# Kernel optimization log

Measured on AMD Instinct MI355X. Metric: run time of the kernel, lower is better.

The kernel has to match this reference:

```python
import jax, jax.numpy as jnp
import numpy as np

NUM_HEADS = 16
D_MODEL = 1024
HEAD_DIM = D_MODEL // NUM_HEADS
SCALE = float(np.sqrt(HEAD_DIM))  # NOTE: original multiplies q by sqrt(head_dim)
EPS = 1e-5


def layernorm(x, g, b):
    # LayerNorm over last dim (head_dim), learnable affine
    mu = jnp.mean(x, axis=-1, keepdims=True)
    var = jnp.mean(jnp.square(x - mu), axis=-1, keepdims=True)
    return (x - mu) * jax.lax.rsqrt(var + EPS) * g + b


def setup_inputs() -> dict:
    key = jax.random.key(0)
    ks = jax.random.split(key, 8)
    B, Nq, Nc = 2, 2048, 2048
    s = 0.02
    return {
        "x_query": jax.random.normal(ks[0], (B, Nq, D_MODEL), jnp.float32),
        "x_context": jax.random.normal(ks[1], (B, Nc, D_MODEL), jnp.float32),
        "Wq": jax.random.normal(ks[2], (D_MODEL, D_MODEL), jnp.float32) * s,
        "Wkv": jax.random.normal(ks[3], (D_MODEL, 2 * D_MODEL), jnp.float32) * s,
        "Wp": jax.random.normal(ks[4], (D_MODEL, D_MODEL), jnp.float32) * s,
        "bp": jnp.zeros((D_MODEL,), jnp.float32),
        "ln_g": jnp.ones((HEAD_DIM,), jnp.float32),
        "ln_b": jnp.zeros((HEAD_DIM,), jnp.float32),
    }


def reference(x_query, x_context, Wq, Wkv, Wp, bp, ln_g, ln_b):
    B, Nq, _ = x_query.shape
    Nc = x_context.shape[1]
    H, D = NUM_HEADS, HEAD_DIM
    # projections
    q = (x_query @ Wq).reshape(B, Nq, H, D).transpose(0, 2, 1, 3)  # b h n d
    kv = (x_context @ Wkv).reshape(B, Nc, 2, H, D)
    k = kv[:, :, 0].transpose(0, 2, 1, 3)  # b h n d
    v = kv[:, :, 1].transpose(0, 2, 1, 3)
    # QK-LayerNorm (shared params)
    q = layernorm(q, ln_g, ln_b)
    k = layernorm(k, ln_g, ln_b)
    # NOTE: faithful to source — q is MULTIPLIED by sqrt(head_dim)
    q = q * SCALE
    attn = jnp.einsum("bhqd,bhkd->bhqk", q, k)
    attn = jax.nn.softmax(attn, axis=-1)
    out = jnp.einsum("bhqk,bhkd->bhqd", attn, v)
    out = out.transpose(0, 2, 1, 3).reshape(B, Nq, H * D)
    return out @ Wp + bp
```

## Files before the change

kernel.cpp:

```cpp
#include <hip/hip_runtime.h>
#include <stdint.h>

#define NUM_HEADS 16
#define HEAD_DIM 64
#define D_MODEL 1024
#define SEQ 2048
#define BATCH 2

typedef unsigned short u16;
typedef _Float16 f16x8 __attribute__((ext_vector_type(8)));
typedef float f32x4 __attribute__((ext_vector_type(4)));

__device__ __forceinline__ u16 f2h(float f) {
    _Float16 h = (_Float16)f;
    return __builtin_bit_cast(u16, h);
}
__device__ __forceinline__ float h2f(u16 h) {
    return (float)__builtin_bit_cast(_Float16, h);
}
__device__ __forceinline__ uint32_t pkrtz(float a, float b) {
    return __builtin_bit_cast(uint32_t, __builtin_amdgcn_cvt_pkrtz(a, b));
}
__device__ __forceinline__ uint32_t pkrtn(float a, float b) {
    return (uint32_t)f2h(a) | ((uint32_t)f2h(b) << 16);
}

__device__ __forceinline__ float ex2(float x) {
#if __has_builtin(__builtin_amdgcn_exp2f)
    return __builtin_amdgcn_exp2f(x);
#else
    float r;
    asm("v_exp_f32 %0, %1" : "=v"(r) : "v"(x));
    return r;
#endif
}

__device__ __forceinline__ f16x8 ld8h(const u16* p) {
    return *reinterpret_cast<const f16x8*>(p);
}

__device__ __forceinline__ void gl_lds16(const void* g, void* l) {
    __builtin_amdgcn_global_load_lds(
        (const __attribute__((address_space(1))) void*)g,
        (__attribute__((address_space(3))) void*)l,
        16, 0, 0);
}

template <int CTRL>
__device__ __forceinline__ float dpp_mov(float x) {
    return __builtin_bit_cast(float,
        __builtin_amdgcn_update_dpp(0, __builtin_bit_cast(int, x), CTRL, 0xf, 0xf, true));
}
__device__ __forceinline__ float rowsum16(float x) {
    x += dpp_mov<0x121>(x);
    x += dpp_mov<0x122>(x);
    x += dpp_mov<0x124>(x);
    x += dpp_mov<0x128>(x);
    return x;
}

__global__ __launch_bounds__(256) void k_prep(const float* __restrict__ xq,
                                              const float* __restrict__ xc,
                                              const float* __restrict__ Wq,
                                              const float* __restrict__ Wkv,
                                              const float* __restrict__ Wp,
                                              u16* __restrict__ xq16,
                                              u16* __restrict__ xc16,
                                              u16* __restrict__ WqT16,
                                              u16* __restrict__ WkvT16,
                                              u16* __restrict__ WpT16) {
    __shared__ float tile[32][33];
    const int t = blockIdx.x;
    if (t < 8192) {
        int i = t * 256 + threadIdx.x;
        const float* src; u16* dst; int j;
        if (i < 1048576) { src = xq; dst = xq16; j = i; }
        else             { src = xc; dst = xc16; j = i - 1048576; }
        float4 v = reinterpret_cast<const float4*>(src)[j];
        ushort4 o;
        o.x = f2h(v.x); o.y = f2h(v.y); o.z = f2h(v.z); o.w = f2h(v.w);
        reinterpret_cast<ushort4*>(dst)[j] = o;
        return;
    }
    const float* W; u16* WT; int N, bi;
    if (t < 9216)       { W = Wq;  WT = WqT16;  N = 1024; bi = t - 8192; }
    else if (t < 11264) { W = Wkv; WT = WkvT16; N = 2048; bi = t - 9216; }
    else                { W = Wp;  WT = WpT16;  N = 1024; bi = t - 11264; }
    const int K = 1024;
    const int nb = N / 32;
    const int bn = (bi % nb) * 32, bk = (bi / nb) * 32;
    const int tx = threadIdx.x & 31;
    const int ty = threadIdx.x >> 5;
#pragma unroll
    for (int i = 0; i < 32; i += 8)
        tile[ty + i][tx] = W[(size_t)(bk + ty + i) * N + bn + tx];
    __syncthreads();
#pragma unroll
    for (int i = 0; i < 32; i += 8)
        WT[(size_t)(bn + ty + i) * K + bk + tx] = f2h(tile[tx][ty + i]);
}

__device__ __forceinline__ void gemm_mainloop_f16(const u16* __restrict__ A,
                                                  const u16* __restrict__ Bt,
                                                  u16* As, u16* Bs,
                                                  int tileM, int tileN, int K,
                                                  f32x4 acc[4][4]) {
    const int tid = threadIdx.x;
    const int lane = tid & 63;
    const int wv = tid >> 6;
    const int wm = wv >> 1, wn = wv & 1;
    const int quad = lane >> 4, l15 = lane & 15;

    const int c0 = tid, c1 = tid + 256;
    const u16* Ap0 = A + (size_t)(tileM + (c0 >> 2)) * K + (c0 & 3) * 8;
    const u16* Ap1 = A + (size_t)(tileM + (c1 >> 2)) * K + (c1 & 3) * 8;
    const u16* Bp0 = Bt + (size_t)(tileN + (c0 >> 2)) * K + (c0 & 3) * 8;
    const u16* Bp1 = Bt + (size_t)(tileN + (c1 >> 2)) * K + (c1 & 3) * 8;

    gl_lds16(Ap0, &As[c0 * 8]);
    gl_lds16(Ap1, &As[c1 * 8]);
    gl_lds16(Bp0, &Bs[c0 * 8]);
    gl_lds16(Bp1, &Bs[c1 * 8]);

    for (int k0 = 0; k0 < K; k0 += 32) {
        __syncthreads();
        const int cb = (k0 >> 5) & 1;
        if (k0 + 32 < K) {
            const int nbuf = cb ^ 1;
            gl_lds16(Ap0 + k0 + 32, &As[nbuf * 4096 + c0 * 8]);
            gl_lds16(Ap1 + k0 + 32, &As[nbuf * 4096 + c1 * 8]);
            gl_lds16(Bp0 + k0 + 32, &Bs[nbuf * 4096 + c0 * 8]);
            gl_lds16(Bp1 + k0 + 32, &Bs[nbuf * 4096 + c1 * 8]);
        }
        const int cbo = cb * 4096;
        f16x8 af[4], bfr[4];
#pragma unroll
        for (int mi = 0; mi < 4; ++mi)
            af[mi] = ld8h(&As[cbo + (wm * 64 + mi * 16 + l15) * 32 + quad * 8]);
#pragma unroll
        for (int ni = 0; ni < 4; ++ni)
            bfr[ni] = ld8h(&Bs[cbo + (wn * 64 + ni * 16 + l15) * 32 + quad * 8]);
#pragma unroll
        for (int mi = 0; mi < 4; ++mi)
#pragma unroll
            for (int ni = 0; ni < 4; ++ni)
                acc[mi][ni] = __builtin_amdgcn_mfma_f32_16x16x32_f16(
                    af[mi], bfr[ni], acc[mi][ni], 0, 0, 0);
    }
}

#define ACC_INIT()                                                   \
    f32x4 acc[4][4];                                                 \
    _Pragma("unroll") for (int i = 0; i < 4; ++i)                    \
        _Pragma("unroll") for (int j = 0; j < 4; ++j)                \
            acc[i][j] = (f32x4){0.f, 0.f, 0.f, 0.f};

__global__ __launch_bounds__(256, 2) void k_proj_f16(const u16* __restrict__ xq16,
                                                     const u16* __restrict__ xc16,
                                                     const u16* __restrict__ WqT16,
                                                     const u16* __restrict__ WkvT16,
                                                     const float* __restrict__ lng,
                                                     const float* __restrict__ lnb,
                                                     u16* __restrict__ Qh_h,
                                                     u16* __restrict__ Qh_l,
                                                     u16* __restrict__ Kh,
                                                     u16* __restrict__ VT) {
    __shared__ __align__(16) u16 As[2 * 128 * 32];
    __shared__ __align__(16) u16 Bs[2 * 128 * 32];
    const int bx = blockIdx.x;
    const int tileM = blockIdx.y * 128;
    const int tid = threadIdx.x;
    const int lane = tid & 63;
    const int wv = tid >> 6;
    const int wm = wv >> 1, wn = wv & 1;
    const int quad = lane >> 4, l15 = lane & 15;
    ACC_INIT();

    if (bx < 16) {
        const bool isQ = bx < 8;
        const int tileN = (bx & 7) * 128;
        const u16* Axx = isQ ? xq16 : xc16;
        const u16* Bt  = isQ ? WqT16 : WkvT16;
        const float scl = isQ ? 11.5415603294809528f : 1.0f;

        gemm_mainloop_f16(Axx, Bt, As, Bs, tileM, tileN, D_MODEL, acc);

        float gv[4], bv[4];
#pragma unroll
        for (int ni = 0; ni < 4; ++ni) { gv[ni] = lng[ni * 16 + l15]; bv[ni] = lnb[ni * 16 + l15]; }

#pragma unroll
        for (int mi = 0; mi < 4; ++mi) {
#pragma unroll
            for (int r = 0; r < 4; ++r) {
                float sum = 0.f, sq = 0.f;
#pragma unroll
                for (int ni = 0; ni < 4; ++ni) { float x = acc[mi][ni][r]; sum += x; sq += x * x; }
                sum = rowsum16(sum);
                sq  = rowsum16(sq);
                float mu = sum * (1.f / 64.f);
                float var = sq * (1.f / 64.f) - mu * mu;
                float rs = rsqrtf(var + 1e-5f);
                int m = tileM + wm * 64 + mi * 16 + quad * 4 + r;
                int bb = m >> 11, n = m & (SEQ - 1);
#pragma unroll
                for (int ni = 0; ni < 4; ++ni) {
                    int colg = tileN + wn * 64 + ni * 16 + l15;
                    int h = colg >> 6;
                    float y = ((acc[mi][ni][r] - mu) * rs * gv[ni] + bv[ni]) * scl;
                    size_t idx = (((size_t)bb * NUM_HEADS + h) * SEQ + n) * HEAD_DIM + (colg & 63);
                    u16 yh = f2h(y);
                    if (isQ) {
                        Qh_h[idx] = yh;
                        Qh_l[idx] = f2h(y - h2f(yh));
                    } else {
                        Kh[idx] = yh;
                    }
                }
            }
        }
    } else {
        const int tileN = D_MODEL + (bx - 16) * 128;
        gemm_mainloop_f16(xc16, WkvT16, As, Bs, tileM, tileN, D_MODEL, acc);
#pragma unroll
        for (int mi = 0; mi < 4; ++mi) {
            int m0 = tileM + wm * 64 + mi * 16 + quad * 4;
            int bb = m0 >> 11, n0 = m0 & (SEQ - 1);
#pragma unroll
            for (int ni = 0; ni < 4; ++ni) {
                int colg = tileN + wn * 64 + ni * 16 + l15 - D_MODEL;
                int h = colg >> 6, d = colg & 63;
                ushort4 o;
                o.x = f2h(acc[mi][ni][0]);
                o.y = f2h(acc[mi][ni][1]);
                o.z = f2h(acc[mi][ni][2]);
                o.w = f2h(acc[mi][ni][3]);
                *reinterpret_cast<ushort4*>(
                    &VT[(((size_t)bb * NUM_HEADS + h) * HEAD_DIM + d) * SEQ + n0]) = o;
            }
        }
    }
}

__global__ __launch_bounds__(256, 2) void k_gemm_out(const u16* __restrict__ A,
                                                     const u16* __restrict__ Bt,
                                                     const float* __restrict__ bp,
                                                     float* __restrict__ out) {
    __shared__ __align__(16) u16 As[2 * 128 * 32];
    __shared__ __align__(16) u16 Bs[2 * 128 * 32];
    const int tileM = blockIdx.y * 128, tileN = blockIdx.x * 128;
    const int tid = threadIdx.x;
    const int lane = tid & 63;
    const int wv = tid >> 6;
    const int wm = wv >> 1, wn = wv & 1;
    const int quad = lane >> 4, l15 = lane & 15;
    ACC_INIT();
    gemm_mainloop_f16(A, Bt, As, Bs, tileM, tileN, D_MODEL, acc);

    float bpv[4];
#pragma unroll
    for (int ni = 0; ni < 4; ++ni) bpv[ni] = bp[tileN + wn * 64 + ni * 16 + l15];
#pragma unroll
    for (int mi = 0; mi < 4; ++mi) {
#pragma unroll
        for (int r = 0; r < 4; ++r) {
            int m = tileM + wm * 64 + mi * 16 + quad * 4 + r;
#pragma unroll
            for (int ni = 0; ni < 4; ++ni) {
                int colg = tileN + wn * 64 + ni * 16 + l15;
                out[(size_t)m * D_MODEL + colg] = acc[mi][ni][r] + bpv[ni];
            }
        }
    }
}

__global__ __launch_bounds__(256) void k_attn(const u16* __restrict__ Qh_h,
                                              const u16* __restrict__ Qh_l,
                                              const u16* __restrict__ Kh,
                                              const u16* __restrict__ VT,
                                              u16* __restrict__ AO) {
    __shared__ __align__(16) u16 Ks[2 * 64 * 64];
    __shared__ __align__(16) u16 Vs[2 * 64 * 64];
    __shared__ __align__(16) u16 Ps[64 * 64];

    const int tid = threadIdx.x;
    const int lane = tid & 63;
    const int wv = tid >> 6;
    const int quad = lane >> 4, l15 = lane & 15;
    const int sw = l15 & 3;
    const int w1 = (l15 >> 2) & 1;
    const int id = blockIdx.x;
    const int bh = (id & 7) | (((id >> 8) & 3) << 3);
    const int qt = (id >> 3) & 31;

    const size_t bh_off = (size_t)bh * SEQ * HEAD_DIM;
    const u16* Vbh = VT + (size_t)bh * HEAD_DIM * SEQ;

    f16x8 qfh[2], qfl[2];
#pragma unroll
    for (int kt = 0; kt < 2; ++kt) {
        size_t off = bh_off + (size_t)(qt * 64 + wv * 16 + l15) * HEAD_DIM + kt * 32 + quad * 8;
        qfh[kt] = ld8h(Qh_h + off);
        qfl[kt] = ld8h(Qh_l + off);
    }

    f16x8 ones;
#pragma unroll
    for (int i = 0; i < 8; ++i) ones[i] = (_Float16)1.0f;

    const int rr = lane >> 3;
    const int ss = lane & 7;
    const int cc = ss ^ rr;
    const int row0 = wv * 16 + rr;
    const u16* k0 = Kh + bh_off + (size_t)row0 * HEAD_DIM + cc * 8;
    const u16* v0 = Vbh + (size_t)row0 * SEQ + cc * 8;
    const int ldsW = (wv * 16) * 64;

    f32x4 acc_o[4];
    f32x4 acc_l = (f32x4){0.f, 0.f, 0.f, 0.f};
    float m_i = -3.0e38f;
#pragma unroll
    for (int ni = 0; ni < 4; ++ni) acc_o[ni] = (f32x4){0.f, 0.f, 0.f, 0.f};

    gl_lds16(k0,                &Ks[ldsW]);
    gl_lds16(k0 + 8 * HEAD_DIM, &Ks[ldsW + 8 * 64]);
    gl_lds16(v0,                &Vs[ldsW]);
    gl_lds16(v0 + 8 * SEQ,      &Vs[ldsW + 8 * 64]);

    const int psRow = (wv * 16 + l15) * 64;
    const int psW = psRow + (quad ^ (w1 << 1)) * 4;

    for (int j = 0; j < SEQ / 64; ++j) {
        __syncthreads();
        if (j + 1 < SEQ / 64) {
            const int nb = (j + 1) & 1;
            const size_t ko = (size_t)(j + 1) * 64 * HEAD_DIM;
            const int vo = (j + 1) * 64;
            gl_lds16(k0 + ko,                &Ks[nb * 4096 + ldsW]);
            gl_lds16(k0 + ko + 8 * HEAD_DIM, &Ks[nb * 4096 + ldsW + 8 * 64]);
            gl_lds16(v0 + vo,                &Vs[nb * 4096 + ldsW]);
            gl_lds16(v0 + vo + 8 * SEQ,      &Vs[nb * 4096 + ldsW + 8 * 64]);
        }
        const int bb = (j & 1) * 4096;

        f32x4 acc_s[4];
#pragma unroll
        for (int ni = 0; ni < 4; ++ni) acc_s[ni] = (f32x4){0.f, 0.f, 0.f, 0.f};
#pragma unroll
        for (int kt = 0; kt < 2; ++kt) {
            f16x8 kf[4];
#pragma unroll
            for (int ni = 0; ni < 4; ++ni) {
                int slot = (kt * 4 + quad) ^ (l15 & 7);
                kf[ni] = ld8h(&Ks[bb + (ni * 16 + l15) * 64 + slot * 8]);
            }
#pragma unroll
            for (int ni = 0; ni < 4; ++ni) {
                acc_s[ni] = __builtin_amdgcn_mfma_f32_16x16x32_f16(
                    kf[ni], qfh[kt], acc_s[ni], 0, 0, 0);
                acc_s[ni] = __builtin_amdgcn_mfma_f32_16x16x32_f16(
                    kf[ni], qfl[kt], acc_s[ni], 0, 0, 0);
            }
        }

        float mn[4];
#pragma unroll
        for (int ni = 0; ni < 4; ++ni)
            mn[ni] = fmaxf(fmaxf(acc_s[ni][0], acc_s[ni][1]),
                           fmaxf(acc_s[ni][2], acc_s[ni][3]));
        float mx = fmaxf(fmaxf(mn[0], mn[1]), fmaxf(mn[2], mn[3]));
        mx = fmaxf(mx, __shfl_xor(mx, 16, 64));
        mx = fmaxf(mx, __shfl_xor(mx, 32, 64));
        float mnew = fmaxf(m_i, mx);
        if (__any(mx > m_i)) {
            float alpha = ex2(m_i - mnew);
#pragma unroll
            for (int ni = 0; ni < 4; ++ni) acc_o[ni] *= alpha;
            acc_l[0] *= alpha;
            m_i = mnew;
        }
#pragma unroll
        for (int ni = 0; ni < 4; ++ni) {
            float p0 = ex2(acc_s[ni][0] - mnew);
            float p1 = ex2(acc_s[ni][1] - mnew);
            float p2 = ex2(acc_s[ni][2] - mnew);
            float p3 = ex2(acc_s[ni][3] - mnew);
            uint2 u;
            u.x = pkrtz(p0, p1);
            u.y = pkrtz(p2, p3);
            *reinterpret_cast<uint2*>(&Ps[psW + ((ni ^ sw) * 16)]) = u;
        }

#pragma unroll
        for (int kt = 0; kt < 2; ++kt) {
            int pchunk = (kt * 2 + (quad >> 1)) ^ sw;
            f16x8 pf = ld8h(&Ps[psRow + pchunk * 16 + (((quad & 1) ^ w1) * 8)]);
            f16x8 vf[4];
#pragma unroll
            for (int ni = 0; ni < 4; ++ni) {
                int slot = (kt * 4 + quad) ^ (l15 & 7);
                vf[ni] = ld8h(&Vs[bb + (ni * 16 + l15) * 64 + slot * 8]);
            }
#pragma unroll
            for (int ni = 0; ni < 4; ++ni)
                acc_o[ni] = __builtin_amdgcn_mfma_f32_16x16x32_f16(
                    vf[ni], pf, acc_o[ni], 0, 0, 0);
            acc_l = __builtin_amdgcn_mfma_f32_16x16x32_f16(
                ones, pf, acc_l, 0, 0, 0);
        }
    }

    const float inv = 1.0f / acc_l[0];
#pragma unroll
    for (int ni = 0; ni < 4; ++ni) {
        uint2 u;
        u.x = pkrtn(acc_o[ni][0] * inv, acc_o[ni][1] * inv);
        u.y = pkrtn(acc_o[ni][2] * inv, acc_o[ni][3] * inv);
        *reinterpret_cast<uint2*>(&Ps[psW + ((ni ^ sw) * 16)]) = u;
    }
    const int b = bh >> 4, h = bh & 15;
    const int qrow = qt * 64 + wv * 16 + l15;
    const int echunk = quad ^ sw;
    uint4 o0 = *reinterpret_cast<const uint4*>(&Ps[psRow + echunk * 16 + w1 * 8]);
    uint4 o1 = *reinterpret_cast<const uint4*>(&Ps[psRow + echunk * 16 + (1 - w1) * 8]);
    size_t outb = ((size_t)(b * SEQ + qrow)) * D_MODEL + h * 64 + quad * 16;
    *reinterpret_cast<uint4*>(&AO[outb])     = o0;
    *reinterpret_cast<uint4*>(&AO[outb + 8]) = o1;
}

extern "C" void kernel_launch(void* const* d_in, const int* in_sizes, int n_in,
                              void* d_out, int out_size, void* d_ws, size_t ws_size,
                              hipStream_t stream) {
    const float* xq  = (const float*)d_in[0];
    const float* xc  = (const float*)d_in[1];
    const float* Wq  = (const float*)d_in[2];
    const float* Wkv = (const float*)d_in[3];
    const float* Wp  = (const float*)d_in[4];
    const float* bp  = (const float*)d_in[5];
    const float* lng = (const float*)d_in[6];
    const float* lnb = (const float*)d_in[7];
    float* out = (float*)d_out;

    char* ws = (char*)d_ws;
    const size_t MB = 1 << 20;
    u16* xq16   = (u16*)(ws + 0 * MB);
    u16* xc16   = (u16*)(ws + 8 * MB);
    u16* WqT16  = (u16*)(ws + 16 * MB);
    u16* WkvT16 = (u16*)(ws + 18 * MB);
    u16* WpT16  = (u16*)(ws + 22 * MB);
    u16* Qh_h   = (u16*)(ws + 24 * MB);
    u16* Qh_l   = (u16*)(ws + 32 * MB);
    u16* Kh     = (u16*)(ws + 40 * MB);
    u16* VT     = (u16*)(ws + 48 * MB);
    u16* AO     = xq16;

    k_prep<<<12288, 256, 0, stream>>>(xq, xc, Wq, Wkv, Wp,
                                      xq16, xc16, WqT16, WkvT16, WpT16);
    k_proj_f16<<<dim3(24, 32), 256, 0, stream>>>(xq16, xc16, WqT16, WkvT16,
                                                 lng, lnb, Qh_h, Qh_l, Kh, VT);
    k_attn<<<1024, 256, 0, stream>>>(Qh_h, Qh_l, Kh, VT, AO);
    k_gemm_out<<<dim3(8, 32), 256, 0, stream>>>(AO, WpT16, bp, out);
}
```

Baseline: 241.4 us.

## Process 128 query rows per attention block to reuse K/V tiles

Each wave in the attention kernel now handles two 16-row query sub-tiles, so every block covers 128 query rows and the grid shrinks from 1024 to 512 blocks. Each K/V tile loaded into LDS and each K/V fragment read from it feeds twice as many MFMAs, which halves K/V global and LDS traffic per query. The trade-off is more registers per wave (two sets of accumulators, Q fragments and running maxima), a larger P buffer in LDS, and fewer blocks, which may reduce occupancy and leave some of the 256 CUs with uneven work.

```diff
diff --git a/kernel.cpp b/kernel.cpp
--- a/kernel.cpp
+++ b/kernel.cpp
@@ -281,7 +281,7 @@
                                               u16* __restrict__ AO) {
     __shared__ __align__(16) u16 Ks[2 * 64 * 64];
     __shared__ __align__(16) u16 Vs[2 * 64 * 64];
-    __shared__ __align__(16) u16 Ps[64 * 64];
+    __shared__ __align__(16) u16 Ps[128 * 64];
 
     const int tid = threadIdx.x;
     const int lane = tid & 63;
@@ -290,19 +290,22 @@
     const int sw = l15 & 3;
     const int w1 = (l15 >> 2) & 1;
     const int id = blockIdx.x;
-    const int bh = (id & 7) | (((id >> 8) & 3) << 3);
-    const int qt = (id >> 3) & 31;
+    const int bh = (id & 7) | (((id >> 7) & 3) << 3);
+    const int qt = (id >> 3) & 15;
 
     const size_t bh_off = (size_t)bh * SEQ * HEAD_DIM;
     const u16* Vbh = VT + (size_t)bh * HEAD_DIM * SEQ;
 
-    f16x8 qfh[2], qfl[2];
-#pragma unroll
-    for (int kt = 0; kt < 2; ++kt) {
-        size_t off = bh_off + (size_t)(qt * 64 + wv * 16 + l15) * HEAD_DIM + kt * 32 + quad * 8;
-        qfh[kt] = ld8h(Qh_h + off);
-        qfl[kt] = ld8h(Qh_l + off);
-    }
+    f16x8 qfh[2][2], qfl[2][2];
+#pragma unroll
+    for (int h = 0; h < 2; ++h)
+#pragma unroll
+        for (int kt = 0; kt < 2; ++kt) {
+            size_t off = bh_off +
+                (size_t)(qt * 128 + wv * 32 + h * 16 + l15) * HEAD_DIM + kt * 32 + quad * 8;
+            qfh[h][kt] = ld8h(Qh_h + off);
+            qfl[h][kt] = ld8h(Qh_l + off);
+        }
 
     f16x8 ones;
 #pragma unroll
@@ -316,19 +319,23 @@
     const u16* v0 = Vbh + (size_t)row0 * SEQ + cc * 8;
     const int ldsW = (wv * 16) * 64;
 
-    f32x4 acc_o[4];
-    f32x4 acc_l = (f32x4){0.f, 0.f, 0.f, 0.f};
-    float m_i = -3.0e38f;
-#pragma unroll
-    for (int ni = 0; ni < 4; ++ni) acc_o[ni] = (f32x4){0.f, 0.f, 0.f, 0.f};
+    f32x4 acc_o[2][4];
+    f32x4 acc_l0 = (f32x4){0.f, 0.f, 0.f, 0.f};
+    f32x4 acc_l1 = (f32x4){0.f, 0.f, 0.f, 0.f};
+    float m0 = -3.0e38f, m1 = -3.0e38f;
+#pragma unroll
+    for (int h = 0; h < 2; ++h)
+#pragma unroll
+        for (int ni = 0; ni < 4; ++ni) acc_o[h][ni] = (f32x4){0.f, 0.f, 0.f, 0.f};
 
     gl_lds16(k0,                &Ks[ldsW]);
     gl_lds16(k0 + 8 * HEAD_DIM, &Ks[ldsW + 8 * 64]);
     gl_lds16(v0,                &Vs[ldsW]);
     gl_lds16(v0 + 8 * SEQ,      &Vs[ldsW + 8 * 64]);
 
-    const int psRow = (wv * 16 + l15) * 64;
-    const int psW = psRow + (quad ^ (w1 << 1)) * 4;
+    const int psRow0 = (wv * 32 + l15) * 64;
+    const int psRow1 = psRow0 + 16 * 64;
+    const int psX = (quad ^ (w1 << 1)) * 4;
 
     for (int j = 0; j < SEQ / 64; ++j) {
         __syncthreads();
@@ -343,9 +350,12 @@
         }
         const int bb = (j & 1) * 4096;
 
-        f32x4 acc_s[4];
-#pragma unroll
-        for (int ni = 0; ni < 4; ++ni) acc_s[ni] = (f32x4){0.f, 0.f, 0.f, 0.f};
+        f32x4 s0[4], s1[4];
+#pragma unroll
+        for (int ni = 0; ni < 4; ++ni) {
+            s0[ni] = (f32x4){0.f, 0.f, 0.f, 0.f};
+            s1[ni] = (f32x4){0.f, 0.f, 0.f, 0.f};
+        }
 #pragma unroll
         for (int kt = 0; kt < 2; ++kt) {
             f16x8 kf[4];
@@ -356,45 +366,60 @@
             }
 #pragma unroll
             for (int ni = 0; ni < 4; ++ni) {
-                acc_s[ni] = __builtin_amdgcn_mfma_f32_16x16x32_f16(
-                    kf[ni], qfh[kt], acc_s[ni], 0, 0, 0);
-                acc_s[ni] = __builtin_amdgcn_mfma_f32_16x16x32_f16(
-                    kf[ni], qfl[kt], acc_s[ni], 0, 0, 0);
-            }
-        }
-
-        float mn[4];
-#pragma unroll
-        for (int ni = 0; ni < 4; ++ni)
-            mn[ni] = fmaxf(fmaxf(acc_s[ni][0], acc_s[ni][1]),
-                           fmaxf(acc_s[ni][2], acc_s[ni][3]));
-        float mx = fmaxf(fmaxf(mn[0], mn[1]), fmaxf(mn[2], mn[3]));
-        mx = fmaxf(mx, __shfl_xor(mx, 16, 64));
-        mx = fmaxf(mx, __shfl_xor(mx, 32, 64));
-        float mnew = fmaxf(m_i, mx);
-        if (__any(mx > m_i)) {
-            float alpha = ex2(m_i - mnew);
-#pragma unroll
-            for (int ni = 0; ni < 4; ++ni) acc_o[ni] *= alpha;
-            acc_l[0] *= alpha;
-            m_i = mnew;
+                s0[ni] = __builtin_amdgcn_mfma_f32_16x16x32_f16(
+                    kf[ni], qfh[0][kt], s0[ni], 0, 0, 0);
+                s0[ni] = __builtin_amdgcn_mfma_f32_16x16x32_f16(
+                    kf[ni], qfl[0][kt], s0[ni], 0, 0, 0);
+                s1[ni] = __builtin_amdgcn_mfma_f32_16x16x32_f16(
+                    kf[ni], qfh[1][kt], s1[ni], 0, 0, 0);
+                s1[ni] = __builtin_amdgcn_mfma_f32_16x16x32_f16(
+                    kf[ni], qfl[1][kt], s1[ni], 0, 0, 0);
+            }
+        }
+
+        float mxa[2];
+#pragma unroll
+        for (int h = 0; h < 2; ++h) {
+            const f32x4* sh = h ? s1 : s0;
+            float a = fmaxf(fmaxf(sh[0][0], sh[0][1]), fmaxf(sh[0][2], sh[0][3]));
+            float b = fmaxf(fmaxf(sh[1][0], sh[1][1]), fmaxf(sh[1][2], sh[1][3]));
+            float c = fmaxf(fmaxf(sh[2][0], sh[2][1]), fmaxf(sh[2][2], sh[2][3]));
+            float d = fmaxf(fmaxf(sh[3][0], sh[3][1]), fmaxf(sh[3][2], sh[3][3]));
+            float mx = fmaxf(fmaxf(a, b), fmaxf(c, d));
+            mx = fmaxf(mx, __shfl_xor(mx, 16, 64));
+            mx = fmaxf(mx, __shfl_xor(mx, 32, 64));
+            mxa[h] = mx;
+        }
+        float mnew0 = fmaxf(m0, mxa[0]);
+        float mnew1 = fmaxf(m1, mxa[1]);
+        if (__any(fmaxf(mxa[0] - m0, mxa[1] - m1) > 0.f)) {
+            float a0 = ex2(m0 - mnew0);
+            float a1 = ex2(m1 - mnew1);
+#pragma unroll
+            for (int ni = 0; ni < 4; ++ni) { acc_o[0][ni] *= a0; acc_o[1][ni] *= a1; }
+            acc_l0[0] *= a0;
+            acc_l1[0] *= a1;
+            m0 = mnew0;
+            m1 = mnew1;
         }
 #pragma unroll
         for (int ni = 0; ni < 4; ++ni) {
-            float p0 = ex2(acc_s[ni][0] - mnew);
-            float p1 = ex2(acc_s[ni][1] - mnew);
-            float p2 = ex2(acc_s[ni][2] - mnew);
-            float p3 = ex2(acc_s[ni][3] - mnew);
             uint2 u;
-            u.x = pkrtz(p0, p1);
-            u.y = pkrtz(p2, p3);
-            *reinterpret_cast<uint2*>(&Ps[psW + ((ni ^ sw) * 16)]) = u;
+            u.x = pkrtz(ex2(s0[ni][0] - mnew0), ex2(s0[ni][1] - mnew0));
+            u.y = pkrtz(ex2(s0[ni][2] - mnew0), ex2(s0[ni][3] - mnew0));
+            *reinterpret_cast<uint2*>(&Ps[psRow0 + psX + ((ni ^ sw) * 16)]) = u;
+            uint2 v;
+            v.x = pkrtz(ex2(s1[ni][0] - mnew1), ex2(s1[ni][1] - mnew1));
+            v.y = pkrtz(ex2(s1[ni][2] - mnew1), ex2(s1[ni][3] - mnew1));
+            *reinterpret_cast<uint2*>(&Ps[psRow1 + psX + ((ni ^ sw) * 16)]) = v;
         }
 
 #pragma unroll
         for (int kt = 0; kt < 2; ++kt) {
             int pchunk = (kt * 2 + (quad >> 1)) ^ sw;
-            f16x8 pf = ld8h(&Ps[psRow + pchunk * 16 + (((quad & 1) ^ w1) * 8)]);
+            int poff = pchunk * 16 + (((quad & 1) ^ w1) * 8);
+            f16x8 pf0 = ld8h(&Ps[psRow0 + poff]);
+            f16x8 pf1 = ld8h(&Ps[psRow1 + poff]);
             f16x8 vf[4];
 #pragma unroll
             for (int ni = 0; ni < 4; ++ni) {
@@ -402,30 +427,38 @@
                 vf[ni] = ld8h(&Vs[bb + (ni * 16 + l15) * 64 + slot * 8]);
             }
 #pragma unroll
-            for (int ni = 0; ni < 4; ++ni)
-                acc_o[ni] = __builtin_amdgcn_mfma_f32_16x16x32_f16(
-                    vf[ni], pf, acc_o[ni], 0, 0, 0);
-            acc_l = __builtin_amdgcn_mfma_f32_16x16x32_f16(
-                ones, pf, acc_l, 0, 0, 0);
-        }
-    }
-
-    const float inv = 1.0f / acc_l[0];
-#pragma unroll
-    for (int ni = 0; ni < 4; ++ni) {
-        uint2 u;
-        u.x = pkrtn(acc_o[ni][0] * inv, acc_o[ni][1] * inv);
-        u.y = pkrtn(acc_o[ni][2] * inv, acc_o[ni][3] * inv);
-        *reinterpret_cast<uint2*>(&Ps[psW + ((ni ^ sw) * 16)]) = u;
-    }
-    const int b = bh >> 4, h = bh & 15;
-    const int qrow = qt * 64 + wv * 16 + l15;
+            for (int ni = 0; ni < 4; ++ni) {
+                acc_o[0][ni] = __builtin_amdgcn_mfma_f32_16x16x32_f16(
+                    vf[ni], pf0, acc_o[0][ni], 0, 0, 0);
+                acc_o[1][ni] = __builtin_amdgcn_mfma_f32_16x16x32_f16(
+                    vf[ni], pf1, acc_o[1][ni], 0, 0, 0);
+            }
+            acc_l0 = __builtin_amdgcn_mfma_f32_16x16x32_f16(ones, pf0, acc_l0, 0, 0, 0);
+            acc_l1 = __builtin_amdgcn_mfma_f32_16x16x32_f16(ones, pf1, acc_l1, 0, 0, 0);
+        }
+    }
+
+    const int b = bh >> 4, hh = bh & 15;
     const int echunk = quad ^ sw;
-    uint4 o0 = *reinterpret_cast<const uint4*>(&Ps[psRow + echunk * 16 + w1 * 8]);
-    uint4 o1 = *reinterpret_cast<const uint4*>(&Ps[psRow + echunk * 16 + (1 - w1) * 8]);
-    size_t outb = ((size_t)(b * SEQ + qrow)) * D_MODEL + h * 64 + quad * 16;
-    *reinterpret_cast<uint4*>(&AO[outb])     = o0;
-    *reinterpret_cast<uint4*>(&AO[outb + 8]) = o1;
+#pragma unroll
+    for (int h = 0; h < 2; ++h) {
+        const float inv = 1.0f / (h ? acc_l1[0] : acc_l0[0]);
+        const int psRow = h ? psRow1 : psRow0;
+        const f32x4* ao = acc_o[h];
+#pragma unroll
+        for (int ni = 0; ni < 4; ++ni) {
+            uint2 u;
+            u.x = pkrtn(ao[ni][0] * inv, ao[ni][1] * inv);
+            u.y = pkrtn(ao[ni][2] * inv, ao[ni][3] * inv);
+            *reinterpret_cast<uint2*>(&Ps[psRow + psX + ((ni ^ sw) * 16)]) = u;
+        }
+        const int qrow = qt * 128 + wv * 32 + h * 16 + l15;
+        uint4 o0 = *reinterpret_cast<const uint4*>(&Ps[psRow + echunk * 16 + w1 * 8]);
+        uint4 o1 = *reinterpret_cast<const uint4*>(&Ps[psRow + echunk * 16 + (1 - w1) * 8]);
+        size_t outb = ((size_t)(b * SEQ + qrow)) * D_MODEL + hh * 64 + quad * 16;
+        *reinterpret_cast<uint4*>(&AO[outb])     = o0;
+        *reinterpret_cast<uint4*>(&AO[outb + 8]) = o1;
+    }
 }
 
 extern "C" void kernel_launch(void* const* d_in, const int* in_sizes, int n_in,
@@ -458,6 +491,6 @@
                                       xq16, xc16, WqT16, WkvT16, WpT16);
     k_proj_f16<<<dim3(24, 32), 256, 0, stream>>>(xq16, xc16, WqT16, WkvT16,
                                                  lng, lnb, Qh_h, Qh_l, Kh, VT);
-    k_attn<<<1024, 256, 0, stream>>>(Qh_h, Qh_l, Kh, VT, AO);
+    k_attn<<<512, 256, 0, stream>>>(Qh_h, Qh_l, Kh, VT, AO);
     k_gemm_out<<<dim3(8, 32), 256, 0, stream>>>(AO, WpT16, bp, out);
 }
```

Result: faster. 233.3 us (-3.3%).
